# Kernel tuning notes

Measured on AMD Instinct MI355X. Metric: run time of the kernel, lower is better.

Reference implementation:

```python
import jax, jax.numpy as jnp
import numpy as np

T, B, I, H = 512, 64, 512, 512

def _linear_init(key, out_dim, in_dim):
    # torch nn.Linear default init: U(-k, k), k = 1/sqrt(in_dim)
    k1, k2 = jax.random.split(key)
    bound = 1.0 / np.sqrt(in_dim)
    W = jax.random.uniform(k1, (out_dim, in_dim), jnp.float32, -bound, bound)
    b = jax.random.uniform(k2, (out_dim,), jnp.float32, -bound, bound)
    return W, b

def setup_inputs() -> dict:
    key = jax.random.key(0)
    ks = jax.random.split(key, 5)
    inputs = jax.random.normal(ks[0], (T, B, I), jnp.float32)
    Wf, bf = _linear_init(ks[1], H, I + H)
    Wi, bi = _linear_init(ks[2], H, I + H)
    Wg, bg = _linear_init(ks[3], H, I + H)
    Wo, bo = _linear_init(ks[4], H, I + H)
    return {"inputs": inputs, "Wf": Wf, "bf": bf, "Wi": Wi, "bi": bi,
            "Wg": Wg, "bg": bg, "Wo": Wo, "bo": bo}

def reference(inputs, Wf, bf, Wi, bi, Wg, bg, Wo, bo):
    hidden_dim = Wf.shape[0]
    batch = inputs.shape[1]
    h0 = jnp.zeros((batch, hidden_dim), inputs.dtype)
    c0 = jnp.zeros((batch, hidden_dim), inputs.dtype)

    def step(carry, x):
        hx, cx = carry
        comb = jnp.concatenate([x, hx], axis=1)        # [B, I+H]
        f = jax.nn.sigmoid(comb @ Wf.T + bf)
        i = jax.nn.sigmoid(comb @ Wi.T + bi)
        g = jnp.tanh(comb @ Wg.T + bg)
        o = jax.nn.sigmoid(comb @ Wo.T + bo)
        cx = f * cx + i * g
        hx = o * jnp.tanh(cx)
        return (hx, cx), hx

    (hx, cx), outputs = jax.lax.scan(step, (h0, c0), inputs)
    return outputs, hx, cx
```

## Files before the change

### kernel.cpp

```cpp
#include <hip/hip_runtime.h>
#include <hip/hip_bf16.h>
#include <stdint.h>
#include <stddef.h>


#define T_STEPS 512
#define BATCH   64
#define HDIM    512

using short8 = __attribute__((ext_vector_type(8))) short;
using f32x4  = __attribute__((ext_vector_type(4))) float;
using int4v  = __attribute__((ext_vector_type(4))) int;

__device__ __forceinline__ void gload_lds16(const void* g, void* l) {
  __builtin_amdgcn_global_load_lds((const __attribute__((address_space(1))) void*)g,
                                   (__attribute__((address_space(3))) void*)l, 16, 0, 0);
}
__device__ __forceinline__ float sigf(float x) { return 1.0f / (1.0f + __expf(-x)); }
__device__ __forceinline__ float tanh_fast(float x) {
  x = fminf(fmaxf(x, -15.0f), 15.0f);
  float e = __expf(2.0f * x);
  return (e - 1.0f) / (e + 1.0f);
}
__device__ __forceinline__ short bfb(float f) {
  __hip_bfloat16 h = __float2bfloat16(f);
  short s; __builtin_memcpy(&s, &h, 2); return s;
}
__device__ __forceinline__ unsigned bfbits(float f) {
  __hip_bfloat16 h = __float2bfloat16(f);
  unsigned short s; __builtin_memcpy(&s, &h, 2); return (unsigned)s;
}
__device__ __forceinline__ float bf2f(unsigned u) {
  return __builtin_bit_cast(float, u << 16);
}

__global__ __launch_bounds__(256) void k_prep(
    const float* __restrict__ Wf, const float* __restrict__ bf_,
    const float* __restrict__ Wi, const float* __restrict__ bi,
    const float* __restrict__ Wg, const float* __restrict__ bg,
    const float* __restrict__ Wo, const float* __restrict__ bo,
    __hip_bfloat16* __restrict__ wxbt, __hip_bfloat16* __restrict__ whbt,
    float* __restrict__ bias, __hip_bfloat16* __restrict__ hbuf, int* __restrict__ flags)
{
  int idx = blockIdx.x * 256 + threadIdx.x;
  int row = idx >> 9;
  int k   = idx & 511;
  int g = row >> 9, r = row & 511;
  const float* W = (g == 0) ? Wf : (g == 1) ? Wi : (g == 2) ? Wg : Wo;
  const float* B = (g == 0) ? bf_ : (g == 1) ? bi : (g == 2) ? bg : bo;
  wxbt[(size_t)row * 512 + k] = __float2bfloat16(W[(size_t)r * 1024 + k]);
  whbt[(size_t)row * 512 + k] = __float2bfloat16(W[(size_t)r * 1024 + 512 + k]);
  if (k == 0) bias[row] = B[r];
  if (idx < 2 * BATCH * HDIM) hbuf[idx] = __float2bfloat16(0.0f);
  if (idx < 128) flags[idx] = 0;
}

__global__ __launch_bounds__(256) void k_convx(const float* __restrict__ x,
                                               __hip_bfloat16* __restrict__ xbf)
{
  int idx = blockIdx.x * 256 + threadIdx.x;
  const float4* p = (const float4*)x + (size_t)idx * 2;
  float4 a = p[0], b = p[1];
  short8 o;
  o[0]=bfb(a.x); o[1]=bfb(a.y); o[2]=bfb(a.z); o[3]=bfb(a.w);
  o[4]=bfb(b.x); o[5]=bfb(b.y); o[6]=bfb(b.z); o[7]=bfb(b.w);
  *(short8*)((short*)xbf + (size_t)idx * 8) = o;
}

__global__ __launch_bounds__(256) void k_xproj(
    const __hip_bfloat16* __restrict__ xbf,
    const __hip_bfloat16* __restrict__ wxbt,
    const float* __restrict__ bias,
    __hip_bfloat16* __restrict__ xproj)
{
  __shared__ __align__(16) short aT[128 * 64];
  __shared__ __align__(16) short bT[128 * 64];
  const int tid = threadIdx.x, lane = tid & 63, wave = tid >> 6;
  const int m0 = blockIdx.y * 128, n0 = blockIdx.x * 128;
  const int wr = wave >> 1, wc = wave & 1;

  f32x4 acc[4][4] = {};

  for (int s = 0; s < 8; ++s) {
    __syncthreads();
    const int kbyte = s * 128;
#pragma unroll
    for (int it = 0; it < 4; ++it) {
      int flat = it * 256 + tid;
      int row = flat >> 3, gr = flat & 7;
      int sgr = gr ^ (row & 7);
      const char* ga = (const char*)xbf  + (size_t)(m0 + row) * 1024 + kbyte + sgr * 16;
      const char* gb = (const char*)wxbt + (size_t)(n0 + row) * 1024 + kbyte + sgr * 16;
      gload_lds16(ga, (char*)aT + (it * 256 + wave * 64) * 16);
      gload_lds16(gb, (char*)bT + (it * 256 + wave * 64) * 16);
    }
    __syncthreads();
#pragma unroll
    for (int kk2 = 0; kk2 < 2; ++kk2) {
      short8 af[4], bfr[4];
#pragma unroll
      for (int mt = 0; mt < 4; ++mt) {
        int r = wr * 64 + mt * 16 + (lane & 15);
        int g = (kk2 * 4 + (lane >> 4)) ^ (r & 7);
        af[mt] = *(const short8*)((const char*)aT + r * 128 + g * 16);
      }
#pragma unroll
      for (int nt = 0; nt < 4; ++nt) {
        int r = wc * 64 + nt * 16 + (lane & 15);
        int g = (kk2 * 4 + (lane >> 4)) ^ (r & 7);
        bfr[nt] = *(const short8*)((const char*)bT + r * 128 + g * 16);
      }
#pragma unroll
      for (int mt = 0; mt < 4; ++mt)
#pragma unroll
        for (int nt = 0; nt < 4; ++nt)
          acc[mt][nt] = __builtin_amdgcn_mfma_f32_16x16x32_bf16(af[mt], bfr[nt], acc[mt][nt], 0, 0, 0);
    }
  }
#pragma unroll
  for (int nt = 0; nt < 4; ++nt) {
    int n = n0 + wc * 64 + nt * 16 + (lane & 15);
    float bv = bias[n];
    int j2 = (n >> 4) & 31, g2 = n >> 9, c2 = n & 15;
#pragma unroll
    for (int mt = 0; mt < 4; ++mt)
#pragma unroll
      for (int i = 0; i < 4; ++i) {
        int m = m0 + wr * 64 + mt * 16 + (lane >> 4) * 4 + i;
        int tt = m >> 6, rr = m & 63;
        xproj[(((size_t)tt * 32 + j2) * 64 + rr) * 64 + g2 * 16 + c2] =
            __float2bfloat16(acc[mt][nt][i] + bv);
      }
  }
}

__global__ __launch_bounds__(64, 1) void k_recur(
    const __hip_bfloat16* __restrict__ xproj,
    const __hip_bfloat16* __restrict__ whbt,
    __hip_bfloat16* __restrict__ hbuf,
    float* __restrict__ out,
    int* __restrict__ flags)
{
  const int lane = threadIdx.x;
  const int bid  = blockIdx.x;
  const int j = bid >> 2, w = bid & 3;
  const int hc0 = j * 16, col = lane & 15, q = lane >> 4, mrow = q * 4;

  float c_state[4] = {0.f, 0.f, 0.f, 0.f};
  float* out_hx = out + (size_t)T_STEPS * BATCH * HDIM;
  float* out_cx = out_hx + BATCH * HDIM;

  const char* wbase = (const char*)whbt + ((size_t)(hc0 + col)) * 1024 + q * 16;

  for (int t = 0; t < T_STEPS; ++t) {
    const int cur = t & 1;
    short8 bw[16][4];
#pragma unroll
    for (int kk = 0; kk < 16; ++kk)
#pragma unroll
      for (int gg = 0; gg < 4; ++gg)
        bw[kk][gg] = *(const short8*)(wbase + (size_t)gg * 524288 + (size_t)kk * 64);

    const char* xpb = (const char*)xproj +
        (((size_t)t * 32 + j) * 4096 + (size_t)(w * 16 + mrow) * 64 + col) * 2;
    unsigned xpu[4][4];
#pragma unroll
    for (int g = 0; g < 4; ++g)
#pragma unroll
      for (int i = 0; i < 4; ++i) {
        const void* p = xpb + i * 128 + g * 32;
        asm volatile("global_load_ushort %0, %1, off"
                     : "=v"(xpu[g][i]) : "v"(p) : "memory");
      }
    if (t > 0) {
      const int* fp = flags + w * 32 + (lane & 31);
      int fv;
      do {
        asm volatile("global_load_dword %0, %1, off sc0 sc1\n\ts_waitcnt vmcnt(0)"
                     : "=v"(fv) : "v"(fp) : "memory");
      } while (fv < t);
    }
    const char* hb = (const char*)hbuf + cur * (BATCH * HDIM * 2) +
                     (size_t)(w * 16 + (lane & 15)) * 1024 + q * 16;
    int4v araw[16];
#pragma unroll
    for (int kk = 0; kk < 16; ++kk) {
      const void* p = hb + kk * 64;
      asm volatile("global_load_dwordx4 %0, %1, off sc0 sc1"
                   : "=v"(araw[kk]) : "v"(p) : "memory");
    }
    asm volatile("s_waitcnt vmcnt(0)" ::: "memory");
    __builtin_amdgcn_sched_barrier(0);

    f32x4 acc[4] = {};
#pragma unroll
    for (int kk = 0; kk < 16; ++kk) {
      short8 af = __builtin_bit_cast(short8, araw[kk]);
#pragma unroll
      for (int gg = 0; gg < 4; ++gg)
        acc[gg] = __builtin_amdgcn_mfma_f32_16x16x32_bf16(af, bw[kk][gg], acc[gg], 0, 0, 0);
    }

    float hnv[4], cnv[4];
#pragma unroll
    for (int i = 0; i < 4; ++i) {
      float pf = acc[0][i] + bf2f(xpu[0][i]);
      float pi = acc[1][i] + bf2f(xpu[1][i]);
      float pg = acc[2][i] + bf2f(xpu[2][i]);
      float po = acc[3][i] + bf2f(xpu[3][i]);
      float fg = sigf(pf), ig = sigf(pi), gg2 = tanh_fast(pg), og = sigf(po);
      float cn = fg * c_state[i] + ig * gg2;
      c_state[i] = cn;
      cnv[i] = cn;
      hnv[i] = og * tanh_fast(cn);
    }
    char* hnxt = (char*)hbuf + (cur ^ 1) * (BATCH * HDIM * 2) +
                 ((size_t)(w * 16 + mrow) * 512 + hc0 + col) * 2;
#pragma unroll
    for (int i = 0; i < 4; ++i) {
      unsigned hb16 = bfbits(hnv[i]);
      void* p = hnxt + i * 1024;
      asm volatile("global_store_short %0, %1, off sc0 sc1"
                   :: "v"(p), "v"(hb16) : "memory");
    }
    asm volatile("s_waitcnt vmcnt(0)" ::: "memory");
    if (t < T_STEPS - 1 && lane == 0) {
      int nv = t + 1;
      int* fp2 = flags + w * 32 + j;
      asm volatile("global_store_dword %0, %1, off sc0 sc1"
                   :: "v"(fp2), "v"(nv) : "memory");
    }
    float* outb = out + ((size_t)t * BATCH + w * 16 + mrow) * HDIM + hc0 + col;
#pragma unroll
    for (int i = 0; i < 4; ++i) outb[(size_t)i * HDIM] = hnv[i];
    if (t == T_STEPS - 1) {
#pragma unroll
      for (int i = 0; i < 4; ++i) {
        out_hx[(size_t)(w * 16 + mrow + i) * HDIM + hc0 + col] = hnv[i];
        out_cx[(size_t)(w * 16 + mrow + i) * HDIM + hc0 + col] = cnv[i];
      }
    }
  }
}

extern "C" void kernel_launch(void* const* d_in, const int* in_sizes, int n_in,
                              void* d_out, int out_size, void* d_ws, size_t ws_size,
                              hipStream_t stream) {
  const float* x   = (const float*)d_in[0];
  const float* Wf  = (const float*)d_in[1];
  const float* bf_ = (const float*)d_in[2];
  const float* Wi  = (const float*)d_in[3];
  const float* bi  = (const float*)d_in[4];
  const float* Wg  = (const float*)d_in[5];
  const float* bg  = (const float*)d_in[6];
  const float* Wo  = (const float*)d_in[7];
  const float* bo  = (const float*)d_in[8];

  char* ws = (char*)d_ws;
  __hip_bfloat16* xbf   = (__hip_bfloat16*)(ws);
  __hip_bfloat16* wxbt  = (__hip_bfloat16*)(ws + 33554432);
  __hip_bfloat16* whbt  = (__hip_bfloat16*)(ws + 35651584);
  float*          bias  = (float*)         (ws + 37748736);
  __hip_bfloat16* xproj = (__hip_bfloat16*)(ws + 37756928);
  __hip_bfloat16* hbuf  = (__hip_bfloat16*)(ws + 171974656);
  int*            flags = (int*)           (ws + 172105728);

  k_prep <<<4096, 256, 0, stream>>>(Wf, bf_, Wi, bi, Wg, bg, Wo, bo,
                                    wxbt, whbt, bias, hbuf, flags);
  k_convx<<<8192, 256, 0, stream>>>(x, xbf);
  k_xproj<<<dim3(16, 256), 256, 0, stream>>>(xbf, wxbt, bias, xproj);
  k_recur<<<128, 64, 0, stream>>>(xproj, whbt, hbuf, (float*)d_out, flags);
}
```

Baseline: 1.858 ms.

## Replace per-step flag polling with step-tagged hidden-state words

Drops the separate flag array and its spin loop in the recurrent kernel. Each bf16 hidden value is now stored as a 32-bit word whose high half holds the step number, so consumers poll the hidden-state buffer itself until every tag matches the current step. This removes the store-wait-flag round trip and one dependent load latency per step. In exchange the hidden buffer doubles in size, each poll reads twice as many bytes, and a repack is needed before the MFMA.

```diff
diff --git a/kernel.cpp b/kernel.cpp
--- a/kernel.cpp
+++ b/kernel.cpp
@@ -40,7 +40,7 @@
     const float* __restrict__ Wg, const float* __restrict__ bg,
     const float* __restrict__ Wo, const float* __restrict__ bo,
     __hip_bfloat16* __restrict__ wxbt, __hip_bfloat16* __restrict__ whbt,
-    float* __restrict__ bias, __hip_bfloat16* __restrict__ hbuf, int* __restrict__ flags)
+    float* __restrict__ bias, unsigned* __restrict__ hbuf32)
 {
   int idx = blockIdx.x * 256 + threadIdx.x;
   int row = idx >> 9;
@@ -51,8 +51,7 @@
   wxbt[(size_t)row * 512 + k] = __float2bfloat16(W[(size_t)r * 1024 + k]);
   whbt[(size_t)row * 512 + k] = __float2bfloat16(W[(size_t)r * 1024 + 512 + k]);
   if (k == 0) bias[row] = B[r];
-  if (idx < 2 * BATCH * HDIM) hbuf[idx] = __float2bfloat16(0.0f);
-  if (idx < 128) flags[idx] = 0;
+  if (idx < 2 * BATCH * HDIM) hbuf32[idx] = 0u;
 }
 
 __global__ __launch_bounds__(256) void k_convx(const float* __restrict__ x,
@@ -137,9 +136,8 @@
 __global__ __launch_bounds__(64, 1) void k_recur(
     const __hip_bfloat16* __restrict__ xproj,
     const __hip_bfloat16* __restrict__ whbt,
-    __hip_bfloat16* __restrict__ hbuf,
-    float* __restrict__ out,
-    int* __restrict__ flags)
+    unsigned* __restrict__ hbuf32,
+    float* __restrict__ out)
 {
   const int lane = threadIdx.x;
   const int bid  = blockIdx.x;
@@ -151,6 +149,8 @@
   float* out_cx = out_hx + BATCH * HDIM;
 
   const char* wbase = (const char*)whbt + ((size_t)(hc0 + col)) * 1024 + q * 16;
+  const char* hbl = (const char*)hbuf32 +
+                    ((size_t)(w * 16 + (lane & 15)) * 512 + q * 8) * 4;
 
   for (int t = 0; t < T_STEPS; ++t) {
     const int cur = t & 1;
@@ -172,30 +172,39 @@
         asm volatile("global_load_ushort %0, %1, off"
                      : "=v"(xpu[g][i]) : "v"(p) : "memory");
       }
-    if (t > 0) {
-      const int* fp = flags + w * 32 + (lane & 31);
-      int fv;
-      do {
-        asm volatile("global_load_dword %0, %1, off sc0 sc1\n\ts_waitcnt vmcnt(0)"
-                     : "=v"(fv) : "v"(fp) : "memory");
-      } while (fv < t);
-    }
-    const char* hb = (const char*)hbuf + cur * (BATCH * HDIM * 2) +
-                     (size_t)(w * 16 + (lane & 15)) * 1024 + q * 16;
-    int4v araw[16];
+
+    const char* hb = hbl + (size_t)cur * (BATCH * HDIM * 4);
+    int4v raw[32];
+    unsigned andv;
+    do {
+#pragma unroll
+      for (int kk = 0; kk < 16; ++kk) {
+        const void* p0 = hb + (size_t)kk * 128;
+        const void* p1 = hb + (size_t)kk * 128 + 16;
+        asm volatile("global_load_dwordx4 %0, %1, off sc0 sc1"
+                     : "=v"(raw[2 * kk]) : "v"(p0) : "memory");
+        asm volatile("global_load_dwordx4 %0, %1, off sc0 sc1"
+                     : "=v"(raw[2 * kk + 1]) : "v"(p1) : "memory");
+      }
+      asm volatile("s_waitcnt vmcnt(0)" ::: "memory");
+      __builtin_amdgcn_sched_barrier(0);
+      andv = 0xffffffffu;
+#pragma unroll
+      for (int ii = 0; ii < 32; ++ii)
+        andv &= (unsigned)raw[ii][0] & (unsigned)raw[ii][1]
+              & (unsigned)raw[ii][2] & (unsigned)raw[ii][3];
+    } while ((andv >> 16) != (unsigned)t);
+    __builtin_amdgcn_sched_barrier(0);
+
+    f32x4 acc[4] = {};
 #pragma unroll
     for (int kk = 0; kk < 16; ++kk) {
-      const void* p = hb + kk * 64;
-      asm volatile("global_load_dwordx4 %0, %1, off sc0 sc1"
-                   : "=v"(araw[kk]) : "v"(p) : "memory");
-    }
-    asm volatile("s_waitcnt vmcnt(0)" ::: "memory");
-    __builtin_amdgcn_sched_barrier(0);
-
-    f32x4 acc[4] = {};
-#pragma unroll
-    for (int kk = 0; kk < 16; ++kk) {
-      short8 af = __builtin_bit_cast(short8, araw[kk]);
+      int4v afw;
+      afw[0] = (raw[2*kk][0]   & 0xffff) | (raw[2*kk][1]   << 16);
+      afw[1] = (raw[2*kk][2]   & 0xffff) | (raw[2*kk][3]   << 16);
+      afw[2] = (raw[2*kk+1][0] & 0xffff) | (raw[2*kk+1][1] << 16);
+      afw[3] = (raw[2*kk+1][2] & 0xffff) | (raw[2*kk+1][3] << 16);
+      short8 af = __builtin_bit_cast(short8, afw);
 #pragma unroll
       for (int gg = 0; gg < 4; ++gg)
         acc[gg] = __builtin_amdgcn_mfma_f32_16x16x32_bf16(af, bw[kk][gg], acc[gg], 0, 0, 0);
@@ -214,21 +223,17 @@
       cnv[i] = cn;
       hnv[i] = og * tanh_fast(cn);
     }
-    char* hnxt = (char*)hbuf + (cur ^ 1) * (BATCH * HDIM * 2) +
-                 ((size_t)(w * 16 + mrow) * 512 + hc0 + col) * 2;
-#pragma unroll
-    for (int i = 0; i < 4; ++i) {
-      unsigned hb16 = bfbits(hnv[i]);
-      void* p = hnxt + i * 1024;
-      asm volatile("global_store_short %0, %1, off sc0 sc1"
-                   :: "v"(p), "v"(hb16) : "memory");
-    }
-    asm volatile("s_waitcnt vmcnt(0)" ::: "memory");
-    if (t < T_STEPS - 1 && lane == 0) {
-      int nv = t + 1;
-      int* fp2 = flags + w * 32 + j;
-      asm volatile("global_store_dword %0, %1, off sc0 sc1"
-                   :: "v"(fp2), "v"(nv) : "memory");
+    if (t < T_STEPS - 1) {
+      char* hnxt = (char*)hbuf32 + (size_t)(cur ^ 1) * (BATCH * HDIM * 4) +
+                   ((size_t)(w * 16 + mrow) * 512 + hc0 + col) * 4;
+      unsigned tag = ((unsigned)(t + 1)) << 16;
+#pragma unroll
+      for (int i = 0; i < 4; ++i) {
+        unsigned word = bfbits(hnv[i]) | tag;
+        void* p = hnxt + (size_t)i * 2048;
+        asm volatile("global_store_dword %0, %1, off sc0 sc1"
+                     :: "v"(p), "v"(word) : "memory");
+      }
     }
     float* outb = out + ((size_t)t * BATCH + w * 16 + mrow) * HDIM + hc0 + col;
 #pragma unroll
@@ -262,12 +267,11 @@
   __hip_bfloat16* whbt  = (__hip_bfloat16*)(ws + 35651584);
   float*          bias  = (float*)         (ws + 37748736);
   __hip_bfloat16* xproj = (__hip_bfloat16*)(ws + 37756928);
-  __hip_bfloat16* hbuf  = (__hip_bfloat16*)(ws + 171974656);
-  int*            flags = (int*)           (ws + 172105728);
+  unsigned*       hbuf32= (unsigned*)      (ws + 171974656);
 
   k_prep <<<4096, 256, 0, stream>>>(Wf, bf_, Wi, bi, Wg, bg, Wo, bo,
-                                    wxbt, whbt, bias, hbuf, flags);
+                                    wxbt, whbt, bias, hbuf32);
   k_convx<<<8192, 256, 0, stream>>>(x, xbf);
   k_xproj<<<dim3(16, 256), 256, 0, stream>>>(xbf, wxbt, bias, xproj);
-  k_recur<<<128, 64, 0, stream>>>(xproj, whbt, hbuf, (float*)d_out, flags);
-}
+  k_recur<<<128, 64, 0, stream>>>(xproj, whbt, hbuf32, (float*)d_out);
+}
```

Result: slower. 2.103 ms (+13.2%).
